# Performance work log

Hardware: AMD Instinct MI355X
Metric: run time of the kernel (lower is better)

Reference implementation:

```python
import jax, jax.numpy as jnp
import numpy as np

B_SZ, IN_DIM, N_NEURONS, N_LAYERS, N_OUTS = 65536, 4, 512, 8, 4


def setup_inputs() -> dict:
    key = jax.random.key(0)
    ks = jax.random.split(key, 5)
    glorot = lambda k, shape: jax.random.normal(k, shape, jnp.float32) * np.sqrt(2.0 / (shape[-2] + shape[-1]))
    inputs = jax.random.normal(ks[0], (B_SZ, IN_DIM), jnp.float32)
    # GaussianRFF projection matrix (fixed random Gaussian)
    B_rff = jax.random.normal(ks[1], (IN_DIM, N_NEURONS // 2), jnp.float32)
    Ws = glorot(ks[2], (N_LAYERS, N_NEURONS, N_NEURONS))
    bs = jnp.zeros((N_LAYERS, N_NEURONS), jnp.float32)
    alphas = jnp.zeros((N_LAYERS + 1,), jnp.float32)  # LAAF slopes, init 0
    Wf = glorot(ks[3], (N_NEURONS, N_OUTS))           # final mixer, no bias
    scale = jnp.ones((N_OUTS,), jnp.float32)          # Scaler, no bias
    return {"inputs": inputs, "B_rff": B_rff, "Ws": Ws, "bs": bs,
            "alphas": alphas, "Wf": Wf, "scale": scale}


def _mlp(x, B_rff, Ws, bs, alphas, Wf, scale):
    # Gaussian random Fourier feature embedding -> [B, n_neurons]
    z = x @ B_rff
    u = jnp.concatenate([jnp.sin(z), jnp.cos(z)], axis=-1)
    L = Ws.shape[0]
    def step(u, p):
        W, b, a = p
        # LAAF sine layer: sin(w0 * (1 + alpha) * (uW + b)), w0 = 1.0
        return jnp.sin((1.0 + a) * (u @ W + b)), None
    u, _ = jax.lax.scan(step, u, (Ws, bs, alphas[:L]))
    return (u @ Wf) * scale  # [B, 4] = (A1, A2, A3, phi)


def reference(inputs, B_rff, Ws, bs, alphas, Wf, scale):
    f = lambda x: _mlp(x, B_rff, Ws, bs, alphas, Wf, scale)
    def jvp_col(col):
        tang = jnp.zeros_like(inputs).at[:, col].set(1.0)
        return jax.jvp(f, (inputs,), (tang,))
    # input columns: 0=t, 1=z, 2=x, 3=y
    P, dPdz = jvp_col(1)
    _, dPdx = jvp_col(2)
    _, dPdy = jvp_col(3)
    A1_y, A1_z = dPdy[:, 0:1], dPdz[:, 0:1]
    A2_x, A2_z = dPdx[:, 1:2], dPdz[:, 1:2]
    A3_x, A3_y = dPdx[:, 2:3], dPdy[:, 2:3]
    phi_x, phi_y, phi_z = dPdx[:, 3:4], dPdy[:, 3:4], dPdz[:, 3:4]
    u = (A3_y - A2_z) + phi_x
    v = (A1_z - A3_x) + phi_y
    w = (A2_x - A1_y) + phi_z
    return jnp.concatenate([u, v, w], axis=1)
```

## Files before the change

kernel.cpp:

```cpp
#include <hip/hip_runtime.h>
#include <stdint.h>


#define B_SZ   65536
#define NN     512
#define NL     8
#define SPB    16
#define MROWS  64
#define NKS    32
#define NG2    (NL*NKS)
#define LDS_A  (MROWS*1024)
#define LDS_TOTAL (LDS_A + 1024)

typedef _Float16 f16x8  __attribute__((ext_vector_type(8)));
typedef float    f32x16 __attribute__((ext_vector_type(16)));

__device__ __forceinline__ uint16_t f2h_bits(float f) {
  union { _Float16 h; uint16_t u; } v; v.h = (_Float16)f; return v.u;
}
__device__ __forceinline__ float h2f(uint16_t b) {
  union { uint16_t u; _Float16 h; } v; v.u = b; return (float)v.h;
}

__device__ __forceinline__ int abyte(int m, int k) {
  const int tile = k >> 4, khp = (k >> 3) & 1, e = k & 7;
  const int mp = m ^ (khp << 2) ^ ((tile & 1) << 1);
  return (tile << 11) + (khp << 10) + (mp << 4) + (e << 1);
}

__global__ __launch_bounds__(512) void prep_weights(const float* __restrict__ Ws,
                                                    uint16_t* __restrict__ img) {
  const int g2 = blockIdx.x;
  const int l  = g2 >> 5, ks = g2 & 31;
  const float* src = Ws + ((size_t)l << 18);
  char* dst = (char*)img + ((size_t)g2 << 14);
  #pragma unroll
  for (int it = 0; it < 2; ++it) {
    const int fidx = threadIdx.x + it*512;
    const int ln  = fidx & 63, sub = fidx >> 6;
    const int n     = (sub >> 1)*64 + (sub & 1)*32 + (ln & 31);
    const int kbase = ks*16 + (ln >> 5)*8;
    uint16_t h[8];
    #pragma unroll
    for (int e = 0; e < 8; ++e)
      h[e] = f2h_bits(src[(size_t)(kbase + e)*512 + n]);
    uint4 pk;
    pk.x = (uint32_t)h[0] | ((uint32_t)h[1] << 16);
    pk.y = (uint32_t)h[2] | ((uint32_t)h[3] << 16);
    pk.z = (uint32_t)h[4] | ((uint32_t)h[5] << 16);
    pk.w = (uint32_t)h[6] | ((uint32_t)h[7] << 16);
    *(uint4*)(dst + (size_t)fidx*16) = pk;
  }
}

__global__ __launch_bounds__(512, 4) void pinn_fused(
    const float* __restrict__ inputs, const float* __restrict__ Brff,
    const float* __restrict__ bs, const float* __restrict__ alphas,
    const float* __restrict__ Wf, const float* __restrict__ scl,
    const uint16_t* __restrict__ wimg, float* __restrict__ out)
{
  extern __shared__ char smem[];

  const int tid  = threadIdx.x;
  const int lane = tid & 63;
  const int wv   = tid >> 6;
  const int l31  = lane & 31;
  const int kh   = lane >> 5;
  const int sbase = blockIdx.x * SPB;

  const char* wp  = (const char*)wimg;
  const int  boff = wv*2048 + lane*16;

  const int av0 = (kh << 10) + ((l31 ^ (kh << 2)) << 4);
  const int av1 = av0 ^ 32;

  f16x8 bA0, bA1, bB0, bB1;
  bA0 = *(const f16x8*)(wp + boff);
  bA1 = *(const f16x8*)(wp + boff + 1024);
  bB0 = *(const f16x8*)(wp + 16384 + boff);
  bB1 = *(const f16x8*)(wp + 16384 + boff + 1024);

  {
    const int k = tid, col = k & 255;
    const bool iscos = (k >= 256);
    const float b0 = Brff[col];
    const float b1 = Brff[256 + col];
    const float b2 = Brff[512 + col];
    const float b3 = Brff[768 + col];
    const int cb  = ((k >> 4) << 11) + (((k >> 3) & 1) << 10) + ((k & 7) << 1);
    const int xm  = (((k >> 3) & 1) << 2) ^ (((k >> 4) & 1) << 1);
    for (int s = 0; s < SPB; ++s) {
      const float4 x = *(const float4*)(inputs + ((size_t)(sbase + s) << 2));
      const float z = x.x*b0 + x.y*b1 + x.z*b2 + x.w*b3;
      const float szn = __sinf(z), czn = __cosf(z);
      const float u0 = iscos ? czn : szn;
      const float dz = iscos ? -szn : czn;
      const int m0 = 4*s;
      *(uint16_t*)(smem + cb + (((m0+0) ^ xm) << 4)) = f2h_bits(u0);
      *(uint16_t*)(smem + cb + (((m0+1) ^ xm) << 4)) = f2h_bits(dz*b1);
      *(uint16_t*)(smem + cb + (((m0+2) ^ xm) << 4)) = f2h_bits(dz*b2);
      *(uint16_t*)(smem + cb + (((m0+3) ^ xm) << 4)) = f2h_bits(dz*b3);
    }
  }
  __syncthreads();

  f16x8 aA0, aA1, aB0, aB1;
  aA0 = *(const f16x8*)(smem + av0);
  aA1 = *(const f16x8*)(smem + av0 + 512);

  const f32x16 zz = {0,0,0,0,0,0,0,0,0,0,0,0,0,0,0,0};

#define LDA(d0, d1, kss) do {                                              \
    const int _av = ((kss) & 1) ? av1 : av0;                               \
    d0 = *(const f16x8*)(smem + _av + (kss)*2048);                         \
    d1 = *(const f16x8*)(smem + _av + (kss)*2048 + 512);                   \
  } while (0)
#define LDB(d0, d1, gg) do {                                               \
    int _g = (gg); if (_g > NG2-1) _g = NG2-1;                             \
    const char* _p = wp + ((size_t)_g << 14) + boff;                       \
    d0 = *(const f16x8*)_p;                                                \
    d1 = *(const f16x8*)(_p + 1024);                                       \
  } while (0)
#define MFMAQ(x0, x1, y0, y1) do {                                         \
    __builtin_amdgcn_s_setprio(1);                                         \
    a00 = __builtin_amdgcn_mfma_f32_32x32x16_f16(x0, y0, a00, 0, 0, 0);    \
    a01 = __builtin_amdgcn_mfma_f32_32x32x16_f16(x0, y1, a01, 0, 0, 0);    \
    a10 = __builtin_amdgcn_mfma_f32_32x32x16_f16(x1, y0, a10, 0, 0, 0);    \
    a11 = __builtin_amdgcn_mfma_f32_32x32x16_f16(x1, y1, a11, 0, 0, 0);    \
    __builtin_amdgcn_s_setprio(0);                                         \
  } while (0)

  for (int l = 0; l < NL; ++l) {
    f32x16 a00 = zz, a01 = zz, a10 = zz, a11 = zz;
    const int g2b = l*NKS;

    #pragma unroll
    for (int ks = 0; ks < NKS; ks += 2) {
      LDA(aB0, aB1, ks + 1);
      MFMAQ(aA0, aA1, bA0, bA1);
      LDB(bA0, bA1, g2b + ks + 2);
      if (ks + 2 < NKS) LDA(aA0, aA1, ks + 2);
      MFMAQ(aB0, aB1, bB0, bB1);
      LDB(bB0, bB1, g2b + ks + 3);
    }
    __syncthreads();

    const float opa = 1.0f + alphas[l];
    #pragma unroll
    for (int Nt = 0; Nt < 2; ++Nt) {
      const int nc = wv*64 + Nt*32 + l31;
      const int cb = ((nc >> 4) << 11) + (((nc >> 3) & 1) << 10) + ((nc & 7) << 1);
      const int xm = (((nc >> 3) & 1) << 2) ^ (((nc >> 4) & 1) << 1);
      const float bias = bs[l*NN + nc];
      #pragma unroll
      for (int Mt = 0; Mt < 2; ++Mt) {
        const f32x16 c = (Mt == 0) ? (Nt == 0 ? a00 : a01)
                                   : (Nt == 0 ? a10 : a11);
        #pragma unroll
        for (int j = 0; j < 4; ++j) {
          const float hh = opa * (c[4*j] + bias);
          const float un = __sinf(hh);
          const float fc = opa * __cosf(hh);
          const float vv[4] = { un, fc*c[4*j+1], fc*c[4*j+2], fc*c[4*j+3] };
          const int m0 = Mt*32 + 8*j + 4*kh;
          #pragma unroll
          for (int s = 0; s < 4; ++s) {
            const int m = m0 + s;
            *(uint16_t*)(smem + cb + ((m ^ xm) << 4)) = f2h_bits(vv[s]);
          }
        }
      }
    }
    __syncthreads();

    if (l + 1 < NL) {
      aA0 = *(const f16x8*)(smem + av0);
      aA1 = *(const f16x8*)(smem + av0 + 512);
    }
  }

  float* dp = (float*)(smem + LDS_A);
  const float4 sc4 = *(const float4*)scl;
  for (int rr = 0; rr < MROWS/8; ++rr) {
    const int m = wv*(MROWS/8) + rr;
    float p0 = 0.f, p1 = 0.f, p2 = 0.f, p3 = 0.f;
    #pragma unroll
    for (int j = 0; j < 8; ++j) {
      const int k = lane + j*64;
      float a = h2f(*(const uint16_t*)(smem + abyte(m, k)));
      float4 wf = ((const float4*)Wf)[k];
      p0 += a*wf.x; p1 += a*wf.y; p2 += a*wf.z; p3 += a*wf.w;
    }
    #pragma unroll
    for (int d = 1; d < 64; d <<= 1) {
      p0 += __shfl_xor(p0, d, 64);
      p1 += __shfl_xor(p1, d, 64);
      p2 += __shfl_xor(p2, d, 64);
      p3 += __shfl_xor(p3, d, 64);
    }
    if (lane == 0) {
      float4* o = (float4*)(dp + m*4);
      *o = make_float4(p0*sc4.x, p1*sc4.y, p2*sc4.z, p3*sc4.w);
    }
  }
  __syncthreads();

  if (tid < SPB*3) {
    const int sl = tid / 3, c = tid - sl*3;
    const float* d1 = dp + (sl*4 + 1)*4;
    const float* d2 = dp + (sl*4 + 2)*4;
    const float* d3 = dp + (sl*4 + 3)*4;
    float val;
    if (c == 0)      val = d3[2] - d1[1] + d2[3];
    else if (c == 1) val = d1[0] - d2[2] + d3[3];
    else             val = d2[1] - d3[0] + d1[3];
    out[(size_t)(sbase + sl)*3 + c] = val;
  }
}

extern "C" void kernel_launch(void* const* d_in, const int* in_sizes, int n_in,
                              void* d_out, int out_size, void* d_ws, size_t ws_size,
                              hipStream_t stream) {
  const float* inputs = (const float*)d_in[0];
  const float* Brff   = (const float*)d_in[1];
  const float* Ws     = (const float*)d_in[2];
  const float* bsp    = (const float*)d_in[3];
  const float* alph   = (const float*)d_in[4];
  const float* Wfp    = (const float*)d_in[5];
  const float* sclp   = (const float*)d_in[6];
  uint16_t* wimg = (uint16_t*)d_ws;

  prep_weights<<<NG2, 512, 0, stream>>>(Ws, wimg);
  const int nblocks = B_SZ / SPB;
  pinn_fused<<<nblocks, 512, LDS_TOTAL, stream>>>(inputs, Brff, bsp, alph, Wfp, sclp,
                                                  wimg, (float*)d_out);
}
```

Baseline: 1.519 ms.

## Double rows per block to reuse each weight tile across four M tiles

Raises samples per block from 16 to 32 (128 GEMM rows), so each wave computes four 32-row M tiles per loaded weight fragment instead of two. This halves global weight traffic per row and improves the MFMA-to-load ratio. In exchange, LDS use doubles to about 130KB, accumulator registers double, and occupancy drops to 2 blocks per CU, with the inner loop no longer unrolled.

New measurement: 1.767 ms. +16.4%, slower.

```diff
diff --git a/kernel.cpp b/kernel.cpp
--- a/kernel.cpp
+++ b/kernel.cpp
@@ -5,12 +5,13 @@
 #define B_SZ   65536
 #define NN     512
 #define NL     8
-#define SPB    16
-#define MROWS  64
+#define SPB    32
+#define MROWS  128
+#define MT     4
 #define NKS    32
 #define NG2    (NL*NKS)
 #define LDS_A  (MROWS*1024)
-#define LDS_TOTAL (LDS_A + 1024)
+#define LDS_TOTAL (LDS_A + 2048)
 
 typedef _Float16 f16x8  __attribute__((ext_vector_type(8)));
 typedef float    f32x16 __attribute__((ext_vector_type(16)));
@@ -25,7 +26,7 @@
 __device__ __forceinline__ int abyte(int m, int k) {
   const int tile = k >> 4, khp = (k >> 3) & 1, e = k & 7;
   const int mp = m ^ (khp << 2) ^ ((tile & 1) << 1);
-  return (tile << 11) + (khp << 10) + (mp << 4) + (e << 1);
+  return (tile << 12) + (khp << 11) + (mp << 4) + (e << 1);
 }
 
 __global__ __launch_bounds__(512) void prep_weights(const float* __restrict__ Ws,
@@ -53,7 +54,7 @@
   }
 }
 
-__global__ __launch_bounds__(512, 4) void pinn_fused(
+__global__ __launch_bounds__(512, 2) void pinn_fused(
     const float* __restrict__ inputs, const float* __restrict__ Brff,
     const float* __restrict__ bs, const float* __restrict__ alphas,
     const float* __restrict__ Wf, const float* __restrict__ scl,
@@ -70,9 +71,6 @@
 
   const char* wp  = (const char*)wimg;
   const int  boff = wv*2048 + lane*16;
-
-  const int av0 = (kh << 10) + ((l31 ^ (kh << 2)) << 4);
-  const int av1 = av0 ^ 32;
 
   f16x8 bA0, bA1, bB0, bB1;
   bA0 = *(const f16x8*)(wp + boff);
@@ -87,7 +85,7 @@
     const float b1 = Brff[256 + col];
     const float b2 = Brff[512 + col];
     const float b3 = Brff[768 + col];
-    const int cb  = ((k >> 4) << 11) + (((k >> 3) & 1) << 10) + ((k & 7) << 1);
+    const int cb  = ((k >> 4) << 12) + (((k >> 3) & 1) << 11) + ((k & 7) << 1);
     const int xm  = (((k >> 3) & 1) << 2) ^ (((k >> 4) & 1) << 1);
     for (int s = 0; s < SPB; ++s) {
       const float4 x = *(const float4*)(inputs + ((size_t)(sbase + s) << 2));
@@ -104,44 +102,64 @@
   }
   __syncthreads();
 
-  f16x8 aA0, aA1, aB0, aB1;
-  aA0 = *(const f16x8*)(smem + av0);
-  aA1 = *(const f16x8*)(smem + av0 + 512);
+  const char* paE = smem + ((kh << 11) + ((l31 ^ (kh << 2)) << 4));
+  const char* paO = smem + ((kh << 11) + ((l31 ^ (kh << 2) ^ 2) << 4));
+
+  f16x8 aC[MT], aN[MT];
+  #pragma unroll
+  for (int Mt = 0; Mt < MT; ++Mt)
+    aC[Mt] = *(const f16x8*)(paE + Mt*512);
 
   const f32x16 zz = {0,0,0,0,0,0,0,0,0,0,0,0,0,0,0,0};
-
-#define LDA(d0, d1, kss) do {                                              \
-    const int _av = ((kss) & 1) ? av1 : av0;                               \
-    d0 = *(const f16x8*)(smem + _av + (kss)*2048);                         \
-    d1 = *(const f16x8*)(smem + _av + (kss)*2048 + 512);                   \
-  } while (0)
-#define LDB(d0, d1, gg) do {                                               \
-    int _g = (gg); if (_g > NG2-1) _g = NG2-1;                             \
-    const char* _p = wp + ((size_t)_g << 14) + boff;                       \
-    d0 = *(const f16x8*)_p;                                                \
-    d1 = *(const f16x8*)(_p + 1024);                                       \
-  } while (0)
-#define MFMAQ(x0, x1, y0, y1) do {                                         \
-    __builtin_amdgcn_s_setprio(1);                                         \
-    a00 = __builtin_amdgcn_mfma_f32_32x32x16_f16(x0, y0, a00, 0, 0, 0);    \
-    a01 = __builtin_amdgcn_mfma_f32_32x32x16_f16(x0, y1, a01, 0, 0, 0);    \
-    a10 = __builtin_amdgcn_mfma_f32_32x32x16_f16(x1, y0, a10, 0, 0, 0);    \
-    a11 = __builtin_amdgcn_mfma_f32_32x32x16_f16(x1, y1, a11, 0, 0, 0);    \
-    __builtin_amdgcn_s_setprio(0);                                         \
-  } while (0)
+  f32x16 acc[MT][2];
 
   for (int l = 0; l < NL; ++l) {
-    f32x16 a00 = zz, a01 = zz, a10 = zz, a11 = zz;
+    #pragma unroll
+    for (int Mt = 0; Mt < MT; ++Mt) { acc[Mt][0] = zz; acc[Mt][1] = zz; }
     const int g2b = l*NKS;
-
-    #pragma unroll
-    for (int ks = 0; ks < NKS; ks += 2) {
-      LDA(aB0, aB1, ks + 1);
-      MFMAQ(aA0, aA1, bA0, bA1);
-      LDB(bA0, bA1, g2b + ks + 2);
-      if (ks + 2 < NKS) LDA(aA0, aA1, ks + 2);
-      MFMAQ(aB0, aB1, bB0, bB1);
-      LDB(bB0, bB1, g2b + ks + 3);
+    int aoff = 0;
+
+    #pragma unroll 1
+    for (int t = 0; t < NKS/2; ++t) {
+      #pragma unroll
+      for (int Mt = 0; Mt < MT; ++Mt)
+        aN[Mt] = *(const f16x8*)(paO + aoff + 4096 + Mt*512);
+      __builtin_amdgcn_s_setprio(1);
+      #pragma unroll
+      for (int Mt = 0; Mt < MT; ++Mt) {
+        acc[Mt][0] = __builtin_amdgcn_mfma_f32_32x32x16_f16(aC[Mt], bA0, acc[Mt][0], 0, 0, 0);
+        acc[Mt][1] = __builtin_amdgcn_mfma_f32_32x32x16_f16(aC[Mt], bA1, acc[Mt][1], 0, 0, 0);
+      }
+      __builtin_amdgcn_s_setprio(0);
+      {
+        const int gt = g2b + 2*t + 2;
+        if (gt < NG2) {
+          const char* p = wp + ((size_t)gt << 14) + boff;
+          bA0 = *(const f16x8*)p;
+          bA1 = *(const f16x8*)(p + 1024);
+        }
+      }
+      if (t + 1 < NKS/2) {
+        #pragma unroll
+        for (int Mt = 0; Mt < MT; ++Mt)
+          aC[Mt] = *(const f16x8*)(paE + aoff + 8192 + Mt*512);
+      }
+      __builtin_amdgcn_s_setprio(1);
+      #pragma unroll
+      for (int Mt = 0; Mt < MT; ++Mt) {
+        acc[Mt][0] = __builtin_amdgcn_mfma_f32_32x32x16_f16(aN[Mt], bB0, acc[Mt][0], 0, 0, 0);
+        acc[Mt][1] = __builtin_amdgcn_mfma_f32_32x32x16_f16(aN[Mt], bB1, acc[Mt][1], 0, 0, 0);
+      }
+      __builtin_amdgcn_s_setprio(0);
+      {
+        const int gt = g2b + 2*t + 3;
+        if (gt < NG2) {
+          const char* p = wp + ((size_t)gt << 14) + boff;
+          bB0 = *(const f16x8*)p;
+          bB1 = *(const f16x8*)(p + 1024);
+        }
+      }
+      aoff += 8192;
     }
     __syncthreads();
 
@@ -149,13 +167,12 @@
     #pragma unroll
     for (int Nt = 0; Nt < 2; ++Nt) {
       const int nc = wv*64 + Nt*32 + l31;
-      const int cb = ((nc >> 4) << 11) + (((nc >> 3) & 1) << 10) + ((nc & 7) << 1);
+      const int cb = ((nc >> 4) << 12) + (((nc >> 3) & 1) << 11) + ((nc & 7) << 1);
       const int xm = (((nc >> 3) & 1) << 2) ^ (((nc >> 4) & 1) << 1);
       const float bias = bs[l*NN + nc];
       #pragma unroll
-      for (int Mt = 0; Mt < 2; ++Mt) {
-        const f32x16 c = (Mt == 0) ? (Nt == 0 ? a00 : a01)
-                                   : (Nt == 0 ? a10 : a11);
+      for (int Mt = 0; Mt < MT; ++Mt) {
+        const f32x16 c = acc[Mt][Nt];
         #pragma unroll
         for (int j = 0; j < 4; ++j) {
           const float hh = opa * (c[4*j] + bias);
@@ -174,8 +191,9 @@
     __syncthreads();
 
     if (l + 1 < NL) {
-      aA0 = *(const f16x8*)(smem + av0);
-      aA1 = *(const f16x8*)(smem + av0 + 512);
+      #pragma unroll
+      for (int Mt = 0; Mt < MT; ++Mt)
+        aC[Mt] = *(const f16x8*)(paE + Mt*512);
     }
   }
 
```

## Double-buffer weight tiles in LDS via global_load_lds and double block rows

Applied to the files above, without the earlier changes.

The block now processes 32 samples (128 rows) with 1024 threads in a 2x8 wave grid. Each wave used to read weight fragments straight from global memory into registers. Now each K-tile of weights is staged into one of two LDS buffers with async global_load_lds, and all 16 waves share it. The aim is to halve global and L2 weight traffic per row and overlap weight fetches with MFMA work. The cost is extra barriers per K-step, higher LDS use (160KB) that limits occupancy to one block per CU, and reliance on manual waitcnt ordering.

Measured after the change: 1.755 ms. 15.6% more time.

```diff
diff --git a/kernel.cpp b/kernel.cpp
--- a/kernel.cpp
+++ b/kernel.cpp
@@ -5,12 +5,13 @@
 #define B_SZ   65536
 #define NN     512
 #define NL     8
-#define SPB    16
-#define MROWS  64
+#define SPB    32
+#define MROWS  128
 #define NKS    32
 #define NG2    (NL*NKS)
-#define LDS_A  (MROWS*1024)
-#define LDS_TOTAL (LDS_A + 1024)
+#define LDS_AA (MROWS*1024)
+#define BBUF   16384
+#define LDS_TOTAL (LDS_AA + 2*BBUF)
 
 typedef _Float16 f16x8  __attribute__((ext_vector_type(8)));
 typedef float    f32x16 __attribute__((ext_vector_type(16)));
@@ -25,7 +26,7 @@
 __device__ __forceinline__ int abyte(int m, int k) {
   const int tile = k >> 4, khp = (k >> 3) & 1, e = k & 7;
   const int mp = m ^ (khp << 2) ^ ((tile & 1) << 1);
-  return (tile << 11) + (khp << 10) + (mp << 4) + (e << 1);
+  return (tile << 12) + (khp << 11) + (mp << 4) + (e << 1);
 }
 
 __global__ __launch_bounds__(512) void prep_weights(const float* __restrict__ Ws,
@@ -53,7 +54,7 @@
   }
 }
 
-__global__ __launch_bounds__(512, 4) void pinn_fused(
+__global__ __launch_bounds__(1024, 4) void pinn_fused(
     const float* __restrict__ inputs, const float* __restrict__ Brff,
     const float* __restrict__ bs, const float* __restrict__ alphas,
     const float* __restrict__ Wf, const float* __restrict__ scl,
@@ -64,32 +65,37 @@
   const int tid  = threadIdx.x;
   const int lane = tid & 63;
   const int wv   = tid >> 6;
+  const int wr   = wv >> 3;
+  const int wc   = wv & 7;
   const int l31  = lane & 31;
   const int kh   = lane >> 5;
   const int sbase = blockIdx.x * SPB;
 
-  const char* wp  = (const char*)wimg;
-  const int  boff = wv*2048 + lane*16;
-
-  const int av0 = (kh << 10) + ((l31 ^ (kh << 2)) << 4);
-  const int av1 = av0 ^ 32;
-
-  f16x8 bA0, bA1, bB0, bB1;
-  bA0 = *(const f16x8*)(wp + boff);
-  bA1 = *(const f16x8*)(wp + boff + 1024);
-  bB0 = *(const f16x8*)(wp + 16384 + boff);
-  bB1 = *(const f16x8*)(wp + 16384 + boff + 1024);
+  char* bbuf0 = smem + LDS_AA;
+  char* bbuf1 = bbuf0 + BBUF;
+
+  auto stage = [&](int g2, char* bb) {
+    const char* src = (const char*)wimg + ((size_t)g2 << 14)
+                    + ((size_t)wv << 10) + (size_t)lane * 16;
+    __builtin_amdgcn_global_load_lds(
+        (const __attribute__((address_space(1))) void*)src,
+        (__attribute__((address_space(3))) void*)(bb + (wv << 10)), 16, 0, 0);
+  };
+
+  stage(0, bbuf0);
+  stage(1, bbuf1);
 
   {
-    const int k = tid, col = k & 255;
+    const int k = tid & 511, sh = tid >> 9, col = k & 255;
     const bool iscos = (k >= 256);
     const float b0 = Brff[col];
     const float b1 = Brff[256 + col];
     const float b2 = Brff[512 + col];
     const float b3 = Brff[768 + col];
-    const int cb  = ((k >> 4) << 11) + (((k >> 3) & 1) << 10) + ((k & 7) << 1);
-    const int xm  = (((k >> 3) & 1) << 2) ^ (((k >> 4) & 1) << 1);
-    for (int s = 0; s < SPB; ++s) {
+    const int cb = ((k >> 4) << 12) + (((k >> 3) & 1) << 11) + ((k & 7) << 1);
+    const int xm = (((k >> 3) & 1) << 2) ^ (((k >> 4) & 1) << 1);
+    for (int ss = 0; ss < SPB/2; ++ss) {
+      const int s = sh*(SPB/2) + ss;
       const float4 x = *(const float4*)(inputs + ((size_t)(sbase + s) << 2));
       const float z = x.x*b0 + x.y*b1 + x.z*b2 + x.w*b3;
       const float szn = __sinf(z), czn = __cosf(z);
@@ -104,23 +110,15 @@
   }
   __syncthreads();
 
-  f16x8 aA0, aA1, aB0, aB1;
-  aA0 = *(const f16x8*)(smem + av0);
-  aA1 = *(const f16x8*)(smem + av0 + 512);
-
+  const int bro = wc*2048 + lane*16;
+  const int aoE = (kh << 11) + (((wr << 6) + (l31 ^ (kh << 2))) << 4);
+  const char* paE = smem + aoE;
+  const char* paO = smem + (aoE ^ 32);
+
+  f16x8 aE0, aE1, aO0, aO1, bE0, bE1, bO0, bO1;
   const f32x16 zz = {0,0,0,0,0,0,0,0,0,0,0,0,0,0,0,0};
-
-#define LDA(d0, d1, kss) do {                                              \
-    const int _av = ((kss) & 1) ? av1 : av0;                               \
-    d0 = *(const f16x8*)(smem + _av + (kss)*2048);                         \
-    d1 = *(const f16x8*)(smem + _av + (kss)*2048 + 512);                   \
-  } while (0)
-#define LDB(d0, d1, gg) do {                                               \
-    int _g = (gg); if (_g > NG2-1) _g = NG2-1;                             \
-    const char* _p = wp + ((size_t)_g << 14) + boff;                       \
-    d0 = *(const f16x8*)_p;                                                \
-    d1 = *(const f16x8*)(_p + 1024);                                       \
-  } while (0)
+  f32x16 a00, a01, a10, a11;
+
 #define MFMAQ(x0, x1, y0, y1) do {                                         \
     __builtin_amdgcn_s_setprio(1);                                         \
     a00 = __builtin_amdgcn_mfma_f32_32x32x16_f16(x0, y0, a00, 0, 0, 0);    \
@@ -131,25 +129,51 @@
   } while (0)
 
   for (int l = 0; l < NL; ++l) {
-    f32x16 a00 = zz, a01 = zz, a10 = zz, a11 = zz;
-    const int g2b = l*NKS;
-
-    #pragma unroll
-    for (int ks = 0; ks < NKS; ks += 2) {
-      LDA(aB0, aB1, ks + 1);
-      MFMAQ(aA0, aA1, bA0, bA1);
-      LDB(bA0, bA1, g2b + ks + 2);
-      if (ks + 2 < NKS) LDA(aA0, aA1, ks + 2);
-      MFMAQ(aB0, aB1, bB0, bB1);
-      LDB(bB0, bB1, g2b + ks + 3);
-    }
-    __syncthreads();
+    a00 = zz; a01 = zz; a10 = zz; a11 = zz;
+    const int g2b = l << 5;
+    int atile = 0;
+
+    #pragma unroll 1
+    for (int t = 0; t < NKS/2; ++t) {
+      {
+        asm volatile("s_waitcnt vmcnt(1)" ::: "memory");
+        __builtin_amdgcn_s_barrier();
+        __builtin_amdgcn_sched_barrier(0);
+        bE0 = *(const f16x8*)(bbuf0 + bro);
+        bE1 = *(const f16x8*)(bbuf0 + bro + 1024);
+        aE0 = *(const f16x8*)(paE + atile);
+        aE1 = *(const f16x8*)(paE + atile + 512);
+        if (t) MFMAQ(aO0, aO1, bO0, bO1);
+        asm volatile("s_waitcnt lgkmcnt(0)" ::: "memory");
+        __builtin_amdgcn_s_barrier();
+        __builtin_amdgcn_sched_barrier(0);
+        int gs = g2b + 2*t + 2; if (gs > NG2-1) gs = NG2-1;
+        stage(gs, bbuf0);
+      }
+      {
+        asm volatile("s_waitcnt vmcnt(1)" ::: "memory");
+        __builtin_amdgcn_s_barrier();
+        __builtin_amdgcn_sched_barrier(0);
+        bO0 = *(const f16x8*)(bbuf1 + bro);
+        bO1 = *(const f16x8*)(bbuf1 + bro + 1024);
+        aO0 = *(const f16x8*)(paO + atile + 4096);
+        aO1 = *(const f16x8*)(paO + atile + 4096 + 512);
+        MFMAQ(aE0, aE1, bE0, bE1);
+        asm volatile("s_waitcnt lgkmcnt(0)" ::: "memory");
+        __builtin_amdgcn_s_barrier();
+        __builtin_amdgcn_sched_barrier(0);
+        int gs = g2b + 2*t + 3; if (gs > NG2-1) gs = NG2-1;
+        stage(gs, bbuf1);
+      }
+      atile += 8192;
+    }
+    MFMAQ(aO0, aO1, bO0, bO1);
 
     const float opa = 1.0f + alphas[l];
     #pragma unroll
     for (int Nt = 0; Nt < 2; ++Nt) {
-      const int nc = wv*64 + Nt*32 + l31;
-      const int cb = ((nc >> 4) << 11) + (((nc >> 3) & 1) << 10) + ((nc & 7) << 1);
+      const int nc = wc*64 + Nt*32 + l31;
+      const int cb = ((nc >> 4) << 12) + (((nc >> 3) & 1) << 11) + ((nc & 7) << 1);
       const int xm = (((nc >> 3) & 1) << 2) ^ (((nc >> 4) & 1) << 1);
       const float bias = bs[l*NN + nc];
       #pragma unroll
@@ -162,7 +186,7 @@
           const float un = __sinf(hh);
           const float fc = opa * __cosf(hh);
           const float vv[4] = { un, fc*c[4*j+1], fc*c[4*j+2], fc*c[4*j+3] };
-          const int m0 = Mt*32 + 8*j + 4*kh;
+          const int m0 = wr*64 + Mt*32 + 8*j + 4*kh;
           #pragma unroll
           for (int s = 0; s < 4; ++s) {
             const int m = m0 + s;
@@ -171,18 +195,16 @@
         }
       }
     }
-    __syncthreads();
-
-    if (l + 1 < NL) {
-      aA0 = *(const f16x8*)(smem + av0);
-      aA1 = *(const f16x8*)(smem + av0 + 512);
-    }
-  }
-
-  float* dp = (float*)(smem + LDS_A);
+    asm volatile("s_waitcnt lgkmcnt(0)" ::: "memory");
+  }
+
+  asm volatile("s_waitcnt vmcnt(0)" ::: "memory");
+  __syncthreads();
+
+  float* dp = (float*)bbuf0;
   const float4 sc4 = *(const float4*)scl;
-  for (int rr = 0; rr < MROWS/8; ++rr) {
-    const int m = wv*(MROWS/8) + rr;
+  for (int rr = 0; rr < 8; ++rr) {
+    const int m = wv*8 + rr;
     float p0 = 0.f, p1 = 0.f, p2 = 0.f, p3 = 0.f;
     #pragma unroll
     for (int j = 0; j < 8; ++j) {
@@ -232,6 +254,6 @@
 
   prep_weights<<<NG2, 512, 0, stream>>>(Ws, wimg);
   const int nblocks = B_SZ / SPB;
-  pinn_fused<<<nblocks, 512, LDS_TOTAL, stream>>>(inputs, Brff, bsp, alph, Wfp, sclp,
-                                                  wimg, (float*)d_out);
-}
+  pinn_fused<<<nblocks, 1024, LDS_TOTAL, stream>>>(inputs, Brff, bsp, alph, Wfp, sclp,
+                                                   wimg, (float*)d_out);
+}
```
